# Kernel tuning notes

Measured on AMD Instinct MI355X. Metric: run time of the kernel, lower is better.

## Reference

```python
import jax, jax.numpy as jnp
import numpy as np

BLOCK_DIMS = [(512, 512), (512, 512), (512, 512)]
OUTPUT_SIZE = 10
BATCH = 65536
BN_EPS = 1e-5


def sign_ste(x):
    # Binarize = sign() with straight-through estimator (torch code mutates .data,
    # so autograd sees identity). Forward value is exactly jnp.sign(x).
    return x + jax.lax.stop_gradient(jnp.sign(x) - x)


def setup_inputs() -> dict:
    key = jax.random.key(0)
    ks = jax.random.split(key, 2 + 6 * len(BLOCK_DIMS) + 2)
    it = iter(ks)
    x = jax.random.normal(next(it), (BATCH, BLOCK_DIMS[0][0]), dtype=jnp.float32)
    Ws, bs, gammas, betas = [], [], [], []
    for (din, dout) in BLOCK_DIMS:
        lim = 1.0 / np.sqrt(din)
        Ws.append(jax.random.uniform(next(it), (dout, din), jnp.float32, -lim, lim))
        bs.append(jax.random.uniform(next(it), (dout,), jnp.float32, -lim, lim))
        gammas.append(jnp.ones((dout,), jnp.float32))
        betas.append(jnp.zeros((dout,), jnp.float32))
        next(it); next(it)  # burn keys for determinism symmetry
    din = BLOCK_DIMS[-1][1]
    lim = 1.0 / np.sqrt(din)
    W_out = jax.random.uniform(next(it), (OUTPUT_SIZE, din), jnp.float32, -lim, lim)
    b_out = jax.random.uniform(next(it), (OUTPUT_SIZE,), jnp.float32, -lim, lim)
    return {"x": x, "Ws": Ws, "bs": bs, "gammas": gammas, "betas": betas,
            "W_out": W_out, "b_out": b_out}


def reference(x, Ws, bs, gammas, betas, W_out, b_out):
    # x.view(-1, input_size) then Binarize(x); BinarizeLinear re-binarizes its
    # input (sign is idempotent) and binarizes its weight, keeps float bias.
    h = sign_ste(x)
    for W, b, g, be in zip(Ws, bs, gammas, betas):
        h = jnp.einsum('bi,oi->bo', sign_ste(h), sign_ste(W)) + b
        # BatchNorm1d in training mode: biased batch statistics over the batch dim
        mu = jnp.mean(h, axis=0)
        var = jnp.var(h, axis=0)
        h = (h - mu) * jax.lax.rsqrt(var + BN_EPS) * g + be
        h = jnp.clip(h, -1.0, 1.0)  # Hardtanh
    h = jnp.einsum('bi,oi->bo', sign_ste(h), sign_ste(W_out)) + b_out
    return jax.nn.log_softmax(h, axis=-1)
```

## Files before the change

### kernel.cpp

```cpp
#include <hip/hip_runtime.h>
#include <stdint.h>

typedef unsigned long long u64;
typedef unsigned int u32;

#define BATCH   65536
#define DIN     512
#define NW      8
#define NCLS    10
#define RPB     64
#define NSL     16


__device__ u64 g_bits[2][BATCH * NW];
__device__ u64 g_mask[2][BATCH * NW];
__device__ u64 g_rowflag[2][BATCH / 64];
__device__ int g_colpart[2][NSL][DIN];
__device__ int g_S1[DIN];
__device__ int g_fastflag[4];
__device__ u64 g_wbitsT[NW * DIN];
__device__ u64 g_wmaskT[NW * DIN];
__device__ int g_wz[4];
__device__ u64 g_obits[NCLS * NW];
__device__ u64 g_omask[NCLS * NW];

__global__ __launch_bounds__(512) void k_init(
    const float* __restrict__ g0, const float* __restrict__ b0,
    const float* __restrict__ g1, const float* __restrict__ b1,
    const float* __restrict__ g2, const float* __restrict__ b2,
    const float* __restrict__ Wout)
{
    const int tid = threadIdx.x, bx = blockIdx.x;
    const int t = bx * 512 + tid;
    for (int k = t; k < NSL * DIN; k += 12 * 512)
        ((int*)g_colpart)[k] = 0;
    if (t < BATCH / 64) g_rowflag[0][t] = 0;
    if (t < 4) g_wz[t] = 0;

    if (bx >= 8 && bx <= 10) {
        const float* gp = (bx == 8) ? g0 : (bx == 9) ? g1 : g2;
        const float* bp = (bx == 8) ? b0 : (bx == 9) ? b1 : b2;
        __shared__ int s_ok;
        if (tid == 0) s_ok = 1;
        __syncthreads();
        float g = gp[tid], be = bp[tid];
        bool ok = (g > 0.0f) && (be == 0.0f);
        u64 bal = __ballot(ok);
        if ((tid & 63) == 0 && bal != ~0ull) s_ok = 0;
        __syncthreads();
        if (tid == 0) g_fastflag[bx - 8] = s_ok;
    }
    if (bx == 11 && tid < 128) {
        const int lane = tid & 63, wv = tid >> 6;
        for (int row = wv; row < NCLS; row += 2) {
            const float4* p = (const float4*)(Wout + (size_t)row * DIN + lane * 8);
            float4 v0 = p[0], v1 = p[1];
            float f[8] = {v0.x, v0.y, v0.z, v0.w, v1.x, v1.y, v1.z, v1.w};
            u32 byteS = 0, byteM = 0;
#pragma unroll
            for (int j = 0; j < 8; j++) {
                u32 pos = f[j] > 0.0f;
                u32 nz  = f[j] != 0.0f;
                byteS |= pos << j;
                byteM |= nz << j;
            }
            u64 wS = 0, wM = 0;
            const int src = (lane & 7) * 8;
#pragma unroll
            for (int j = 0; j < 8; j++) {
                wS |= (u64)(__shfl((int)byteS, src + j) & 0xFF) << (8 * j);
                wM |= (u64)(__shfl((int)byteM, src + j) & 0xFF) << (8 * j);
            }
            if (lane < 8) {
                g_obits[row * NW + lane] = wS;
                g_omask[row * NW + lane] = wM;
            }
        }
    }
}

__global__ __launch_bounds__(256) void k_binarize_x(const float* __restrict__ x)
{
    __shared__ int csB[DIN];
    const int tid = threadIdx.x;
    for (int i = tid; i < DIN; i += 256) csB[i] = 0;
    __syncthreads();
    const int lane = tid & 63, wave = tid >> 6;
    const int gw = blockIdx.x * 4 + wave;
    const int nwv = gridDim.x * 4;
    int cs[8];
#pragma unroll
    for (int j = 0; j < 8; j++) cs[j] = 0;

    for (int row = gw; row < BATCH; row += nwv) {
        const float4* p = (const float4*)(x + (size_t)row * DIN + lane * 8);
        float4 v0 = p[0], v1 = p[1];
        float f[8] = {v0.x, v0.y, v0.z, v0.w, v1.x, v1.y, v1.z, v1.w};
        u32 byteS = 0, byteM = 0;
#pragma unroll
        for (int j = 0; j < 8; j++) {
            u32 pos = f[j] > 0.0f;
            u32 nz  = f[j] != 0.0f;
            byteS |= pos << j;
            byteM |= nz << j;
            cs[j] += nz ? (pos ? 1 : -1) : 0;
        }
        u64 wS = 0, wM = 0;
        const int src = (lane & 7) * 8;
#pragma unroll
        for (int j = 0; j < 8; j++) {
            wS |= (u64)(__shfl((int)byteS, src + j) & 0xFF) << (8 * j);
            wM |= (u64)(__shfl((int)byteM, src + j) & 0xFF) << (8 * j);
        }
        if (lane < 8) {
            g_bits[0][(size_t)row * NW + lane] = wS;
            g_mask[0][(size_t)row * NW + lane] = wM;
        }
        u64 ok = __ballot(byteM == 0xFFu);
        if (lane == 0 && ok != ~0ull)
            atomicOr(&g_rowflag[0][row >> 6], 1ull << (row & 63));
    }
#pragma unroll
    for (int j = 0; j < 8; j++)
        if (cs[j]) atomicAdd(&csB[lane * 8 + j], cs[j]);
    __syncthreads();
    for (int i = tid; i < DIN; i += 256) {
        int v = csB[i];
        if (v) atomicAdd(&g_colpart[0][blockIdx.x & (NSL - 1)][i], v);
    }
}

__global__ __launch_bounds__(512) void k_prep_w(const float* __restrict__ W,
                                                int sel, int layer)
{
    const int so = sel ^ 1;
    __shared__ int csL[DIN];
    const int tid = threadIdx.x;
    const int t1 = blockIdx.x * 512 + tid;
    if (t1 < NSL * DIN) ((int*)&g_colpart[so][0][0])[t1] = 0;
    if (t1 < BATCH / 64) g_rowflag[so][t1] = 0;
    {
        int s = 0;
#pragma unroll
        for (int p = 0; p < NSL; p++) s += g_colpart[sel][p][tid];
        csL[tid] = s;
    }
    __syncthreads();
    const int lane = tid & 63, wave = tid >> 6;
    const int gw = blockIdx.x * 8 + wave;
    const int nwv = gridDim.x * 8;
    for (int row = gw; row < DIN; row += nwv) {
        const float4* p = (const float4*)(W + (size_t)row * DIN + lane * 8);
        float4 v0 = p[0], v1 = p[1];
        float f[8] = {v0.x, v0.y, v0.z, v0.w, v1.x, v1.y, v1.z, v1.w};
        u32 byteS = 0, byteM = 0;
        int contrib = 0;
#pragma unroll
        for (int j = 0; j < 8; j++) {
            u32 pos = f[j] > 0.0f;
            u32 nz  = f[j] != 0.0f;
            byteS |= pos << j;
            byteM |= nz << j;
            int s = nz ? (pos ? 1 : -1) : 0;
            contrib += s * csL[lane * 8 + j];
        }
        u64 wS = 0, wM = 0;
        const int src = (lane & 7) * 8;
#pragma unroll
        for (int j = 0; j < 8; j++) {
            wS |= (u64)(__shfl((int)byteS, src + j) & 0xFF) << (8 * j);
            wM |= (u64)(__shfl((int)byteM, src + j) & 0xFF) << (8 * j);
        }
        if (lane < 8) {
            g_wbitsT[(size_t)lane * DIN + row] = wS;
            g_wmaskT[(size_t)lane * DIN + row] = wM;
        }
        u64 ok = __ballot(byteM == 0xFFu);
#pragma unroll
        for (int o = 32; o; o >>= 1) contrib += __shfl_down(contrib, o);
        if (lane == 0) {
            g_S1[row] = contrib;
            if (ok != ~0ull) atomicOr(&g_wz[layer], 1);
        }
    }
}

__global__ __launch_bounds__(256, 4) void k_bingemm(int sel, int layer,
        const float* __restrict__ gamma, const float* __restrict__ beta)
{
    const int so = sel ^ 1;
    __shared__ alignas(16) u64 AT[RPB * NW];
    const int tid  = threadIdx.x;
    const int lane = tid & 63;
    const int wv   = tid >> 6;
    const int rowBase = blockIdx.x * RPB;

    {
        ulonglong2* dst = (ulonglong2*)AT;
        const ulonglong2* src = (const ulonglong2*)&g_bits[sel][(size_t)rowBase * NW];
        dst[tid] = src[tid];
    }
    const int col0 = wv * 128 + lane;
    const int col1 = col0 + 64;
    u64 w0[8], w1[8];
#pragma unroll
    for (int c = 0; c < 8; c++) {
        w0[c] = g_wbitsT[c * DIN + col0];
        w1[c] = g_wbitsT[c * DIN + col1];
    }
    const int thr0 = g_S1[col0];
    const int thr1 = g_S1[col1];
    const int R0 = (DIN << 16) - thr0, R1 = (DIN << 16) - thr1;
    const int tg0 = (R0 + ((1 << 17) - 1)) >> 17, tl0 = (R0 >> 17) + 1;
    const int tg1 = (R1 + ((1 << 17) - 1)) >> 17, tl1 = (R1 >> 17) + 1;
    const u64 rflags = g_rowflag[sel][blockIdx.x];
    const bool slowAll = (g_fastflag[layer] == 0) || (g_wz[layer] != 0);
    int cs0 = 0, cs1 = 0;
    u64 mB0 = 0, mB1 = 0, mM0 = 0, mM1 = 0;
    __syncthreads();

    if (!slowAll && rflags == 0) {
#pragma unroll 4
        for (int r = 0; r < RPB; r++) {
            const ulonglong2* Av = (const ulonglong2*)(AT + r * NW);
            ulonglong2 A0 = Av[0], A1 = Av[1], A2 = Av[2], A3 = Av[3];
            const u64 aw[8] = {A0.x, A0.y, A1.x, A1.y, A2.x, A2.y, A3.x, A3.y};
            int P0 = 0, P1 = 0;
#pragma unroll
            for (int c = 0; c < 8; c++) {
                P0 += __popcll(aw[c] ^ w0[c]);
                P1 += __popcll(aw[c] ^ w1[c]);
            }
            bool gb0 = P0 < tg0, lb0 = P0 >= tl0;
            bool gb1 = P1 < tg1, lb1 = P1 >= tl1;
            u64 gt0 = __ballot(gb0), nz0 = gt0 | __ballot(lb0);
            u64 gt1 = __ballot(gb1), nz1 = gt1 | __ballot(lb1);
            cs0 += (int)gb0 - (int)lb0;
            cs1 += (int)gb1 - (int)lb1;
            bool mine = (lane == r);
            mB0 = mine ? gt0 : mB0;  mB1 = mine ? gt1 : mB1;
            mM0 = mine ? nz0 : mM0;  mM1 = mine ? nz1 : mM1;
            if ((nz0 & nz1) != ~0ull) {
                if (lane == 0)
                    atomicOr(&g_rowflag[so][(rowBase + r) >> 6],
                             1ull << ((rowBase + r) & 63));
            }
        }
    } else {
        double td0 = 0.0, td1 = 0.0;
        int md0 = 0, md1 = 0;
        {
            float g = gamma[col0], be = beta[col0];
            int S1v = thr0;
            td0 = (double)S1v;
            if (g != 0.0f) {
                md0 = (g > 0.0f) ? 0 : 1;
                if (be != 0.0f) {
                    double s = rsqrt((double)DIN + 1e-5);
                    td0 = (double)S1v - 65536.0 * (double)be / (s * (double)g);
                }
            } else md0 = (be > 0.0f) ? 2 : ((be < 0.0f) ? 3 : 4);
            g = gamma[col1]; be = beta[col1]; S1v = thr1;
            td1 = (double)S1v;
            if (g != 0.0f) {
                md1 = (g > 0.0f) ? 0 : 1;
                if (be != 0.0f) {
                    double s = rsqrt((double)DIN + 1e-5);
                    td1 = (double)S1v - 65536.0 * (double)be / (s * (double)g);
                }
            } else md1 = (be > 0.0f) ? 2 : ((be < 0.0f) ? 3 : 4);
        }
        for (int r = 0; r < RPB; r++) {
            int bit0, bit1;
            if (!slowAll && !((rflags >> r) & 1)) {
                int P0 = 0, P1 = 0;
#pragma unroll
                for (int c = 0; c < 8; c++) {
                    u64 a = AT[r * NW + c];
                    P0 += __popcll(a ^ w0[c]);
                    P1 += __popcll(a ^ w1[c]);
                }
                int v0 = (DIN - 2 * P0) << 16;
                int v1 = (DIN - 2 * P1) << 16;
                bit0 = (v0 > thr0) - (v0 < thr0);
                bit1 = (v1 > thr1) - (v1 < thr1);
            } else {
                const int row = rowBase + r;
                int P0 = 0, Q0 = 0, P1 = 0, Q1 = 0;
#pragma unroll
                for (int c = 0; c < 8; c++) {
                    u64 a  = AT[r * NW + c];
                    u64 am = g_mask[sel][(size_t)row * NW + c];
                    u64 m0 = am & g_wmaskT[c * DIN + col0];
                    u64 m1 = am & g_wmaskT[c * DIN + col1];
                    P0 += __popcll((a ^ w0[c]) & m0);  Q0 += __popcll(m0);
                    P1 += __popcll((a ^ w1[c]) & m1);  Q1 += __popcll(m1);
                }
                double Ds0 = (double)(Q0 - 2 * P0) * 65536.0;
                double Ds1 = (double)(Q1 - 2 * P1) * 65536.0;
                int c0 = (Ds0 > td0) ? 1 : ((Ds0 < td0) ? -1 : 0);
                int c1 = (Ds1 > td1) ? 1 : ((Ds1 < td1) ? -1 : 0);
                bit0 = (md0 == 0) ? c0 : (md0 == 1) ? -c0
                     : (md0 == 2) ? 1 : (md0 == 3) ? -1 : 0;
                bit1 = (md1 == 0) ? c1 : (md1 == 1) ? -c1
                     : (md1 == 2) ? 1 : (md1 == 3) ? -1 : 0;
            }
            u64 gt0 = __ballot(bit0 > 0), nz0 = __ballot(bit0 != 0);
            u64 gt1 = __ballot(bit1 > 0), nz1 = __ballot(bit1 != 0);
            cs0 += bit0;
            cs1 += bit1;
            bool mine = (lane == r);
            mB0 = mine ? gt0 : mB0;  mB1 = mine ? gt1 : mB1;
            mM0 = mine ? nz0 : mM0;  mM1 = mine ? nz1 : mM1;
            if ((nz0 & nz1) != ~0ull) {
                if (lane == 0)
                    atomicOr(&g_rowflag[so][(rowBase + r) >> 6],
                             1ull << ((rowBase + r) & 63));
            }
        }
    }

    {
        size_t b = (size_t)(rowBase + lane) * NW + 2 * wv;
        ulonglong2 vb; vb.x = mB0; vb.y = mB1;
        ulonglong2 vm; vm.x = mM0; vm.y = mM1;
        *(ulonglong2*)&g_bits[so][b] = vb;
        *(ulonglong2*)&g_mask[so][b] = vm;
    }
    atomicAdd(&g_colpart[so][blockIdx.x & (NSL - 1)][col0], cs0);
    atomicAdd(&g_colpart[so][blockIdx.x & (NSL - 1)][col1], cs1);
}

__global__ __launch_bounds__(256) void k_final(int sel, const float* __restrict__ bout,
                                               float* __restrict__ out)
{
    __shared__ u64 ob[NCLS * NW], om[NCLS * NW];
    __shared__ float bo[NCLS];
    const int tid = threadIdx.x;
    if (tid < NCLS * NW) { ob[tid] = g_obits[tid]; om[tid] = g_omask[tid]; }
    if (tid < NCLS) bo[tid] = bout[tid];
    __syncthreads();
    const int row = blockIdx.x * 256 + tid;
    const u64* pb = &g_bits[sel][(size_t)row * NW];
    const u64* pm = &g_mask[sel][(size_t)row * NW];
    u64 b[NW], m[NW];
#pragma unroll
    for (int c = 0; c < NW; c++) { b[c] = pb[c]; m[c] = pm[c]; }
    float z[NCLS];
    float mx = -1e30f;
#pragma unroll
    for (int o = 0; o < NCLS; o++) {
        int P = 0, P2 = 0;
#pragma unroll
        for (int c = 0; c < NW; c++) {
            u64 mm = m[c] & om[o * NW + c];
            P  += __popcll((b[c] ^ ob[o * NW + c]) & mm);
            P2 += __popcll(mm);
        }
        float v = (float)(P2 - 2 * P) + bo[o];
        z[o] = v;
        mx = fmaxf(mx, v);
    }
    float s = 0.0f;
#pragma unroll
    for (int o = 0; o < NCLS; o++) s += expf(z[o] - mx);
    float l = logf(s);
    float2* o2 = (float2*)(out + (size_t)row * NCLS);
#pragma unroll
    for (int p = 0; p < 5; p++) {
        float2 v;
        v.x = z[2 * p]     - mx - l;
        v.y = z[2 * p + 1] - mx - l;
        o2[p] = v;
    }
}

extern "C" void kernel_launch(void* const* d_in, const int* in_sizes, int n_in,
                              void* d_out, int out_size, void* d_ws, size_t ws_size,
                              hipStream_t stream)
{
    const float *x = 0, *Wl[3] = {0,0,0}, *gl[3] = {0,0,0}, *bl[3] = {0,0,0};
    const float *Wout = 0, *bout = 0;
    {
        int i = 0;
        x = (const float*)d_in[i++];
        if (i < n_in && in_sizes[i] == 3 * DIN * DIN) {
            for (int l = 0; l < 3; l++) Wl[l] = (const float*)d_in[i] + (size_t)l * DIN * DIN;
            i++;
        } else {
            for (int l = 0; l < 3 && i < n_in; l++) Wl[l] = (const float*)d_in[i++];
        }
        if (i < n_in && in_sizes[i] == 3 * DIN) i++;
        else i += 3;
        if (i < n_in && in_sizes[i] == 3 * DIN) {
            for (int l = 0; l < 3; l++) gl[l] = (const float*)d_in[i] + (size_t)l * DIN;
            i++;
        } else {
            for (int l = 0; l < 3 && i < n_in; l++) gl[l] = (const float*)d_in[i++];
        }
        if (i < n_in && in_sizes[i] == 3 * DIN) {
            for (int l = 0; l < 3; l++) bl[l] = (const float*)d_in[i] + (size_t)l * DIN;
            i++;
        } else {
            for (int l = 0; l < 3 && i < n_in; l++) bl[l] = (const float*)d_in[i++];
        }
        if (i < n_in) Wout = (const float*)d_in[i++];
        if (i < n_in) bout = (const float*)d_in[i++];
    }
    float* out = (float*)d_out;
    (void)out_size; (void)d_ws; (void)ws_size;

    k_init<<<12, 512, 0, stream>>>(gl[0], bl[0], gl[1], bl[1], gl[2], bl[2], Wout);
    k_binarize_x<<<1024, 256, 0, stream>>>(x);
    for (int l = 0; l < 3; l++) {
        int sel = l & 1;
        k_prep_w<<<64, 512, 0, stream>>>(Wl[l], sel, l);
        k_bingemm<<<BATCH / RPB, 256, 0, stream>>>(sel, l, gl[l], bl[l]);
    }
    k_final<<<BATCH / 256, 256, 0, stream>>>(1, bout, out);
}
```

Baseline: 367.9 us.

## Fuse final classifier into last bingemm and skip mask writes for nonzero rows

Merges the output layer and log-softmax into the third bingemm kernel through a template flag, so the layer-3 activation bits and masks stay in shared memory and are never written to or reread from global memory. The mask arrays are now written only for rows that contain zeros, and readers load masks only for flagged rows and otherwise treat them as all ones. The x binarize loop now handles two rows per iteration so more loads are in flight. Costs are more shared memory and a few extra syncs in the last GEMM, plus a correctness dependence on the row flags being consistent with which masks were written.

```diff
diff --git a/kernel.cpp b/kernel.cpp
--- a/kernel.cpp
+++ b/kernel.cpp
@@ -92,9 +92,7 @@
 #pragma unroll
     for (int j = 0; j < 8; j++) cs[j] = 0;
 
-    for (int row = gw; row < BATCH; row += nwv) {
-        const float4* p = (const float4*)(x + (size_t)row * DIN + lane * 8);
-        float4 v0 = p[0], v1 = p[1];
+    auto proc = [&](int row, float4 v0, float4 v1) {
         float f[8] = {v0.x, v0.y, v0.z, v0.w, v1.x, v1.y, v1.z, v1.w};
         u32 byteS = 0, byteM = 0;
 #pragma unroll
@@ -112,13 +110,24 @@
             wS |= (u64)(__shfl((int)byteS, src + j) & 0xFF) << (8 * j);
             wM |= (u64)(__shfl((int)byteM, src + j) & 0xFF) << (8 * j);
         }
-        if (lane < 8) {
+        u64 ok = __ballot(byteM == 0xFFu);
+        if (lane < 8)
             g_bits[0][(size_t)row * NW + lane] = wS;
-            g_mask[0][(size_t)row * NW + lane] = wM;
-        }
-        u64 ok = __ballot(byteM == 0xFFu);
-        if (lane == 0 && ok != ~0ull)
-            atomicOr(&g_rowflag[0][row >> 6], 1ull << (row & 63));
+        if (ok != ~0ull) {
+            if (lane < 8) g_mask[0][(size_t)row * NW + lane] = wM;
+            if (lane == 0)
+                atomicOr(&g_rowflag[0][row >> 6], 1ull << (row & 63));
+        }
+    };
+
+    for (int row = gw; row < BATCH; row += 2 * nwv) {
+        const int rowB = row + nwv;
+        const float4* pA = (const float4*)(x + (size_t)row  * DIN + lane * 8);
+        const float4* pB = (const float4*)(x + (size_t)rowB * DIN + lane * 8);
+        float4 a0 = pA[0], a1 = pA[1];
+        float4 b0 = pB[0], b1 = pB[1];
+        proc(row,  a0, a1);
+        proc(rowB, b0, b1);
     }
 #pragma unroll
     for (int j = 0; j < 8; j++)
@@ -185,11 +194,17 @@
     }
 }
 
+template<int FINAL>
 __global__ __launch_bounds__(256, 4) void k_bingemm(int sel, int layer,
-        const float* __restrict__ gamma, const float* __restrict__ beta)
+        const float* __restrict__ gamma, const float* __restrict__ beta,
+        const float* __restrict__ bout, float* __restrict__ out)
 {
     const int so = sel ^ 1;
     __shared__ alignas(16) u64 AT[RPB * NW];
+    __shared__ u64 AZ[FINAL ? 1 : 4];
+    __shared__ u64 SB[FINAL ? RPB * 9 : 1];
+    __shared__ u64 SM[FINAL ? RPB * 9 : 1];
+    __shared__ float ZR[FINAL ? RPB * 11 : 1];
     const int tid  = threadIdx.x;
     const int lane = tid & 63;
     const int wv   = tid >> 6;
@@ -217,6 +232,7 @@
     const bool slowAll = (g_fastflag[layer] == 0) || (g_wz[layer] != 0);
     int cs0 = 0, cs1 = 0;
     u64 mB0 = 0, mB1 = 0, mM0 = 0, mM1 = 0;
+    u64 anyz = 0;
     __syncthreads();
 
     if (!slowAll && rflags == 0) {
@@ -241,6 +257,7 @@
             mB0 = mine ? gt0 : mB0;  mB1 = mine ? gt1 : mB1;
             mM0 = mine ? nz0 : mM0;  mM1 = mine ? nz1 : mM1;
             if ((nz0 & nz1) != ~0ull) {
+                anyz |= 1ull << r;
                 if (lane == 0)
                     atomicOr(&g_rowflag[so][(rowBase + r) >> 6],
                              1ull << ((rowBase + r) & 63));
@@ -271,8 +288,9 @@
             } else md1 = (be > 0.0f) ? 2 : ((be < 0.0f) ? 3 : 4);
         }
         for (int r = 0; r < RPB; r++) {
+            const bool fl = (rflags >> r) & 1;
             int bit0, bit1;
-            if (!slowAll && !((rflags >> r) & 1)) {
+            if (!slowAll && !fl) {
                 int P0 = 0, P1 = 0;
 #pragma unroll
                 for (int c = 0; c < 8; c++) {
@@ -290,7 +308,7 @@
 #pragma unroll
                 for (int c = 0; c < 8; c++) {
                     u64 a  = AT[r * NW + c];
-                    u64 am = g_mask[sel][(size_t)row * NW + c];
+                    u64 am = fl ? g_mask[sel][(size_t)row * NW + c] : ~0ull;
                     u64 m0 = am & g_wmaskT[c * DIN + col0];
                     u64 m1 = am & g_wmaskT[c * DIN + col1];
                     P0 += __popcll((a ^ w0[c]) & m0);  Q0 += __popcll(m0);
@@ -313,6 +331,7 @@
             mB0 = mine ? gt0 : mB0;  mB1 = mine ? gt1 : mB1;
             mM0 = mine ? nz0 : mM0;  mM1 = mine ? nz1 : mM1;
             if ((nz0 & nz1) != ~0ull) {
+                anyz |= 1ull << r;
                 if (lane == 0)
                     atomicOr(&g_rowflag[so][(rowBase + r) >> 6],
                              1ull << ((rowBase + r) & 63));
@@ -320,58 +339,60 @@
         }
     }
 
-    {
-        size_t b = (size_t)(rowBase + lane) * NW + 2 * wv;
+    if constexpr (FINAL) {
+        SB[lane * 9 + 2 * wv]     = mB0;
+        SB[lane * 9 + 2 * wv + 1] = mB1;
+        SM[lane * 9 + 2 * wv]     = mM0;
+        SM[lane * 9 + 2 * wv + 1] = mM1;
+        __syncthreads();
+        u64 b[NW], m[NW];
+#pragma unroll
+        for (int c = 0; c < NW; c++) { b[c] = SB[lane * 9 + c]; m[c] = SM[lane * 9 + c]; }
+        const int cls0 = (wv < 2) ? wv * 3 : 2 + wv * 2;
+        const int ncl  = (wv < 2) ? 3 : 2;
+        for (int k = 0; k < ncl; k++) {
+            const int o = cls0 + k;
+            int P = 0, P2 = 0;
+#pragma unroll
+            for (int c = 0; c < NW; c++) {
+                u64 om = g_omask[o * NW + c];
+                u64 mm = m[c] & om;
+                P  += __popcll((b[c] ^ g_obits[o * NW + c]) & mm);
+                P2 += __popcll(mm);
+            }
+            ZR[lane * 11 + o] = (float)(P2 - 2 * P) + bout[o];
+        }
+        __syncthreads();
+        if (wv == 0) {
+            float z[NCLS], mx = -1e30f;
+#pragma unroll
+            for (int o = 0; o < NCLS; o++) { z[o] = ZR[lane * 11 + o]; mx = fmaxf(mx, z[o]); }
+            float s = 0.0f;
+#pragma unroll
+            for (int o = 0; o < NCLS; o++) s += expf(z[o] - mx);
+            float l = logf(s);
+            float2* o2 = (float2*)(out + (size_t)(rowBase + lane) * NCLS);
+#pragma unroll
+            for (int p = 0; p < 5; p++) {
+                float2 v;
+                v.x = z[2 * p]     - mx - l;
+                v.y = z[2 * p + 1] - mx - l;
+                o2[p] = v;
+            }
+        }
+    } else {
+        AZ[wv] = anyz;
+        __syncthreads();
+        const u64 rowz = AZ[0] | AZ[1] | AZ[2] | AZ[3];
+        size_t bofs = (size_t)(rowBase + lane) * NW + 2 * wv;
         ulonglong2 vb; vb.x = mB0; vb.y = mB1;
-        ulonglong2 vm; vm.x = mM0; vm.y = mM1;
-        *(ulonglong2*)&g_bits[so][b] = vb;
-        *(ulonglong2*)&g_mask[so][b] = vm;
-    }
-    atomicAdd(&g_colpart[so][blockIdx.x & (NSL - 1)][col0], cs0);
-    atomicAdd(&g_colpart[so][blockIdx.x & (NSL - 1)][col1], cs1);
-}
-
-__global__ __launch_bounds__(256) void k_final(int sel, const float* __restrict__ bout,
-                                               float* __restrict__ out)
-{
-    __shared__ u64 ob[NCLS * NW], om[NCLS * NW];
-    __shared__ float bo[NCLS];
-    const int tid = threadIdx.x;
-    if (tid < NCLS * NW) { ob[tid] = g_obits[tid]; om[tid] = g_omask[tid]; }
-    if (tid < NCLS) bo[tid] = bout[tid];
-    __syncthreads();
-    const int row = blockIdx.x * 256 + tid;
-    const u64* pb = &g_bits[sel][(size_t)row * NW];
-    const u64* pm = &g_mask[sel][(size_t)row * NW];
-    u64 b[NW], m[NW];
-#pragma unroll
-    for (int c = 0; c < NW; c++) { b[c] = pb[c]; m[c] = pm[c]; }
-    float z[NCLS];
-    float mx = -1e30f;
-#pragma unroll
-    for (int o = 0; o < NCLS; o++) {
-        int P = 0, P2 = 0;
-#pragma unroll
-        for (int c = 0; c < NW; c++) {
-            u64 mm = m[c] & om[o * NW + c];
-            P  += __popcll((b[c] ^ ob[o * NW + c]) & mm);
-            P2 += __popcll(mm);
-        }
-        float v = (float)(P2 - 2 * P) + bo[o];
-        z[o] = v;
-        mx = fmaxf(mx, v);
-    }
-    float s = 0.0f;
-#pragma unroll
-    for (int o = 0; o < NCLS; o++) s += expf(z[o] - mx);
-    float l = logf(s);
-    float2* o2 = (float2*)(out + (size_t)row * NCLS);
-#pragma unroll
-    for (int p = 0; p < 5; p++) {
-        float2 v;
-        v.x = z[2 * p]     - mx - l;
-        v.y = z[2 * p + 1] - mx - l;
-        o2[p] = v;
+        *(ulonglong2*)&g_bits[so][bofs] = vb;
+        if ((rowz >> lane) & 1) {
+            ulonglong2 vm; vm.x = mM0; vm.y = mM1;
+            *(ulonglong2*)&g_mask[so][bofs] = vm;
+        }
+        atomicAdd(&g_colpart[so][blockIdx.x & (NSL - 1)][col0], cs0);
+        atomicAdd(&g_colpart[so][blockIdx.x & (NSL - 1)][col1], cs1);
     }
 }
 
@@ -412,10 +433,11 @@
 
     k_init<<<12, 512, 0, stream>>>(gl[0], bl[0], gl[1], bl[1], gl[2], bl[2], Wout);
     k_binarize_x<<<1024, 256, 0, stream>>>(x);
-    for (int l = 0; l < 3; l++) {
+    for (int l = 0; l < 2; l++) {
         int sel = l & 1;
         k_prep_w<<<64, 512, 0, stream>>>(Wl[l], sel, l);
-        k_bingemm<<<BATCH / RPB, 256, 0, stream>>>(sel, l, gl[l], bl[l]);
-    }
-    k_final<<<BATCH / 256, 256, 0, stream>>>(1, bout, out);
+        k_bingemm<0><<<BATCH / RPB, 256, 0, stream>>>(sel, l, gl[l], bl[l], bout, out);
+    }
+    k_prep_w<<<64, 512, 0, stream>>>(Wl[2], 0, 2);
+    k_bingemm<1><<<BATCH / RPB, 256, 0, stream>>>(0, 2, gl[2], bl[2], bout, out);
 }
```

Result: faster. 360.0 us (-2.1%).
